# Kernel tuning notes

Hardware: AMD Instinct MI355X
Metric: run time of the kernel (lower is better)

## Reference

```python
import jax, jax.numpy as jnp
import numpy as np

E = 1024
H = 16
HD = E // H  # 64
R = 8
ALPHA = 32
SCALING = ALPHA / R  # LoRA scaling = 4.0


def _lora_linear(x, W, b, A, B):
    # x: [..., in], W: [out, in], A: [r, in], B: [out, r]
    base = jnp.einsum('...i,oi->...o', x, W) + b
    lora = jnp.einsum('...r,or->...o', jnp.einsum('...i,ri->...r', x, A), B) * SCALING
    return base + lora


def setup_inputs() -> dict:
    key = jax.random.key(0)
    ks = jax.random.split(key, 20)
    L, N = 2048, 2
    d = {}
    d['query'] = jax.random.normal(ks[0], (L, N, E), dtype=jnp.float32)
    d['key_padding_mask'] = jax.random.randint(ks[1], (N, L), 0, 2) > 0
    i = 2
    for p in ('q', 'k', 'v', 'o'):
        d['W' + p] = jax.random.normal(ks[i], (E, E), dtype=jnp.float32) * (E ** -0.5); i += 1
        d['b' + p] = jax.random.normal(ks[i], (E,), dtype=jnp.float32) * 0.01; i += 1
        d['A' + p] = jax.random.normal(ks[i], (R, E), dtype=jnp.float32) * (E ** -0.5); i += 1
        d['B' + p] = jax.random.normal(ks[i], (E, R), dtype=jnp.float32) * 0.01; i += 1
    return d


def reference(query, key_padding_mask, Wq, bq, Aq, Bq, Wk, bk, Ak, Bk,
              Wv, bv, Av, Bv, Wo, bo, Ao, Bo):
    L, N, _ = query.shape
    q = _lora_linear(query, Wq, bq, Aq, Bq)  # [L, N, E]
    k = _lora_linear(query, Wk, bk, Ak, Bk)
    v = _lora_linear(query, Wv, bv, Av, Bv)

    def split_heads(x):  # [L, N, E] -> [N, H, L, HD]
        return x.transpose(1, 0, 2).reshape(N, L, H, HD).transpose(0, 2, 1, 3)

    scale = HD ** -0.5
    qh = split_heads(q) * scale
    kh = split_heads(k)
    vh = split_heads(v)

    logits = jnp.einsum('nhqd,nhkd->nhqk', qh, kh)  # [N, H, L, L]
    dt = logits.dtype
    pad = key_padding_mask[:, None, None, :]  # [N, 1, 1, Lk]
    logits = jnp.where(pad, jnp.finfo(dt).min, logits)
    logits = logits - jnp.max(logits, axis=-1, keepdims=True)
    w = jax.nn.softmax(logits, axis=-1)
    # zero out padded keys then renormalize (faithful to the module)
    w = jnp.where(pad, jnp.zeros((), dt), w)
    denom = jnp.maximum(jnp.sum(w, axis=-1, keepdims=True), jnp.finfo(dt).tiny)
    w = w / denom

    out = jnp.einsum('nhqk,nhkd->nhqd', w, vh)  # [N, H, L, HD]
    out = out.transpose(0, 2, 1, 3).reshape(N, L, E).transpose(1, 0, 2)  # [L, N, E]
    attn_output = _lora_linear(out, Wo, bo, Ao, Bo)

    # average_attn_weights=True path: mean over heads, then permute(1,0,2)
    attn_weights_out = jnp.mean(w, axis=1).transpose(1, 0, 2)  # [Lq, N, Lk]
    return attn_output, attn_weights_out
```

## Files before the change

### kernel.cpp

```cpp
#include <hip/hip_runtime.h>
#include <stdint.h>


typedef __attribute__((ext_vector_type(8))) short short8;
typedef __attribute__((ext_vector_type(4))) float f32x4;

#define LORA_SCALING 4.0f
#define FTINY 1.1754943508222875e-38f

static __device__ __forceinline__ unsigned short f2bf(float f){
  unsigned u = __float_as_uint(f);
  u += 0x7fffu + ((u >> 16) & 1u);
  return (unsigned short)(u >> 16);
}
static __device__ __forceinline__ float bflo(unsigned u){ return __uint_as_float(u << 16); }
static __device__ __forceinline__ float bfhi(unsigned u){ return __uint_as_float(u & 0xffff0000u); }
static __device__ __forceinline__ unsigned pk2(float lo, float hi){
  return (unsigned)f2bf(lo) | ((unsigned)f2bf(hi) << 16);
}

union S8U { short8 v; uint2 u[2]; };

__global__ __launch_bounds__(256) void pack_bf16(const float* __restrict__ src,
                                                 unsigned short* __restrict__ dst)
{
  const size_t i = (size_t)blockIdx.x * 256 + threadIdx.x;
  const float4 f0 = ((const float4*)src)[i*2];
  const float4 f1 = ((const float4*)src)[i*2 + 1];
  ((uint4*)dst)[i] = make_uint4(pk2(f0.x,f0.y), pk2(f0.z,f0.w),
                                pk2(f1.x,f1.y), pk2(f1.z,f1.w));
}

__global__ __launch_bounds__(256) void xa_kernel(const unsigned short* __restrict__ X,
                                                 const float* __restrict__ A,
                                                 float* __restrict__ xa)
{
  __shared__ float red[4][8];
  const int t = blockIdx.x, tid = threadIdx.x;
  const int lane = tid & 63, wid = tid >> 6;

  const uint2 xr = *(const uint2*)(X + (size_t)t*1024 + tid*4);
  const float x0 = bflo(xr.x), x1 = bfhi(xr.x), x2 = bflo(xr.y), x3 = bfhi(xr.y);

  float acc[8];
#pragma unroll
  for (int r = 0; r < 8; ++r) {
    const float4 ar = *(const float4*)(A + (size_t)r*1024 + tid*4);
    acc[r] = x0*ar.x + x1*ar.y + x2*ar.z + x3*ar.w;
  }
#pragma unroll
  for (int r = 0; r < 8; ++r) {
    float v = acc[r];
#pragma unroll
    for (int off = 32; off > 0; off >>= 1) v += __shfl_xor(v, off, 64);
    if (lane == 0) red[wid][r] = v;
  }
  __syncthreads();
  if (tid < 8) xa[(size_t)t*8 + tid] = red[0][tid] + red[1][tid] + red[2][tid] + red[3][tid];
}

__global__ __launch_bounds__(256) void gemm_bf16(
    const unsigned short* __restrict__ Abf,
    const unsigned short* __restrict__ W0bf, const unsigned short* __restrict__ W1bf,
    const unsigned short* __restrict__ W2bf,
    const float* __restrict__ B0, const float* __restrict__ B1, const float* __restrict__ B2,
    const float* __restrict__ xa0, const float* __restrict__ xa1, const float* __restrict__ xa2,
    const float* __restrict__ L0, const float* __restrict__ L1, const float* __restrict__ L2,
    void* __restrict__ C0, void* __restrict__ C1, void* __restrict__ C2,
    int fp32out)
{
  const int z = blockIdx.z;
  const unsigned short* W = (z==0)?W0bf:((z==1)?W1bf:W2bf);
  const float* Bb = (z==0)?B0:((z==1)?B1:B2);
  const float* xa = (z==0)?xa0:((z==1)?xa1:xa2);
  const float* Lb = (z==0)?L0:((z==1)?L1:L2);
  void*        C  = (z==0)?C0:((z==1)?C1:C2);
  const bool vtw = (z == 2);

  __shared__ alignas(16) unsigned short As[128*32];
  __shared__ alignas(16) unsigned short Bs[128*32];

  const int tid = threadIdx.x;
  const int lane = tid & 63, wid = tid >> 6;
  const int quad = lane >> 4, lm = lane & 15;
  const int t0 = blockIdx.x * 128, n0 = blockIdx.y * 128;
  const int wm = (wid & 1) * 64, wn = (wid >> 1) * 64;

  const int srow = tid >> 1;
  const int shalf = (tid & 1) * 16;

  f32x4 acc[4][4];
#pragma unroll
  for (int i = 0; i < 4; ++i)
#pragma unroll
    for (int j = 0; j < 4; ++j) acc[i][j] = 0.f;

  for (int kt = 0; kt < 32; ++kt) {
    const int k0 = kt * 32;
    const unsigned short* ga = Abf + (size_t)(t0 + srow)*1024 + k0 + shalf;
    const uint4 a0 = *(const uint4*)ga;
    const uint4 a1 = *(const uint4*)(ga + 8);
    const unsigned short* gb = W + (size_t)(n0 + srow)*1024 + k0 + shalf;
    const uint4 b0 = *(const uint4*)gb;
    const uint4 b1 = *(const uint4*)(gb + 8);
    __syncthreads();
    *(uint4*)&As[srow*32 + shalf]     = a0;
    *(uint4*)&As[srow*32 + shalf + 8] = a1;
    *(uint4*)&Bs[srow*32 + shalf]     = b0;
    *(uint4*)&Bs[srow*32 + shalf + 8] = b1;
    __syncthreads();
    short8 a[4], b[4];
#pragma unroll
    for (int i = 0; i < 4; ++i) a[i] = *(const short8*)&As[(wm + i*16 + lm)*32 + quad*8];
#pragma unroll
    for (int j = 0; j < 4; ++j) b[j] = *(const short8*)&Bs[(wn + j*16 + lm)*32 + quad*8];
#pragma unroll
    for (int i = 0; i < 4; ++i)
#pragma unroll
      for (int j = 0; j < 4; ++j)
        acc[i][j] = __builtin_amdgcn_mfma_f32_16x16x32_bf16(a[i], b[j], acc[i][j], 0, 0, 0);
  }

#pragma unroll
  for (int j = 0; j < 4; ++j) {
    const int col = n0 + wn + j*16 + lm;
    const float bias = Bb[col];
    const float4 u0 = ((const float4*)(Lb + (size_t)col*8))[0];
    const float4 u1 = ((const float4*)(Lb + (size_t)col*8))[1];
#pragma unroll
    for (int i = 0; i < 4; ++i) {
#pragma unroll
      for (int r = 0; r < 4; ++r) {
        const int row = t0 + wm + i*16 + quad*4 + r;
        const float* xr = xa + (size_t)row*8;
        const float lora = xr[0]*u0.x + xr[1]*u0.y + xr[2]*u0.z + xr[3]*u0.w
                         + xr[4]*u1.x + xr[5]*u1.y + xr[6]*u1.z + xr[7]*u1.w;
        const float val = acc[i][j][r] + bias + LORA_SCALING*lora;
        if (fp32out) {
          ((float*)C)[(size_t)row*1024 + col] = val;
        } else if (vtw) {
          ((unsigned short*)C)[((size_t)(row & 1) * 1024 + col) * 2048 + (row >> 1)] = f2bf(val);
        } else {
          ((unsigned short*)C)[(size_t)row*1024 + col] = f2bf(val);
        }
      }
    }
  }
}

__global__ __launch_bounds__(256) void attn_pv(
    const unsigned short* __restrict__ qb, const unsigned short* __restrict__ kb,
    const unsigned short* __restrict__ vt, const int* __restrict__ mask,
    unsigned short* __restrict__ ctx, float* __restrict__ msl)
{
  __shared__ alignas(16) unsigned short Es[128*132];
  __shared__ unsigned char mlds[2048];
  __shared__ float lred[2][128];

  const int tid = threadIdx.x, lane = tid & 63, wid = tid >> 6;
  const int quad = lane >> 4, lm = lane & 15;
  const int q0 = blockIdx.x * 128, n = blockIdx.y, h = blockIdx.z;
  const int wq = wid >> 1, wj = wid & 1;

  {
    const int4 m0 = *(const int4*)(mask + n*2048 + tid*8);
    const int4 m1 = *(const int4*)(mask + n*2048 + tid*8 + 4);
    mlds[tid*8+0] = (m0.x != 0); mlds[tid*8+1] = (m0.y != 0);
    mlds[tid*8+2] = (m0.z != 0); mlds[tid*8+3] = (m0.w != 0);
    mlds[tid*8+4] = (m1.x != 0); mlds[tid*8+5] = (m1.y != 0);
    mlds[tid*8+6] = (m1.z != 0); mlds[tid*8+7] = (m1.w != 0);
  }

  short8 bq[4][2];
#pragma unroll
  for (int q_t = 0; q_t < 4; ++q_t) {
    const unsigned short* qg = qb + ((size_t)(q0 + wq*64 + q_t*16 + lm)*2 + n)*1024 + h*64 + quad*8;
    bq[q_t][0] = *(const short8*)qg;
    bq[q_t][1] = *(const short8*)(qg + 32);
  }

  float lsum[4] = {0.f, 0.f, 0.f, 0.f};
  f32x4 oacc[2][4];
#pragma unroll
  for (int i2 = 0; i2 < 2; ++i2)
#pragma unroll
    for (int dt = 0; dt < 4; ++dt) oacc[i2][dt] = 0.f;

  for (int jt = 0; jt < 16; ++jt) {
    const int j0 = jt * 128;
    __syncthreads();

    f32x4 sacc[4][4];
#pragma unroll
    for (int a = 0; a < 4; ++a)
#pragma unroll
      for (int b = 0; b < 4; ++b) sacc[a][b] = 0.f;
#pragma unroll
    for (int kt = 0; kt < 2; ++kt) {
      short8 ak[4];
#pragma unroll
      for (int j_t = 0; j_t < 4; ++j_t)
        ak[j_t] = *(const short8*)(kb + ((size_t)(j0 + wj*64 + j_t*16 + lm)*2 + n)*1024 + h*64 + kt*32 + quad*8);
#pragma unroll
      for (int j_t = 0; j_t < 4; ++j_t)
#pragma unroll
        for (int q_t = 0; q_t < 4; ++q_t)
          sacc[j_t][q_t] = __builtin_amdgcn_mfma_f32_16x16x32_bf16(ak[j_t], bq[q_t][kt], sacc[j_t][q_t], 0, 0, 0);
    }
#pragma unroll
    for (int j_t = 0; j_t < 4; ++j_t) {
      const int jrow = wj*64 + j_t*16 + quad*4;
      const uchar4 mk = *(const uchar4*)&mlds[j0 + jrow];
#pragma unroll
      for (int q_t = 0; q_t < 4; ++q_t) {
        const float e0 = mk.x ? 0.f : __expf(sacc[j_t][q_t][0]*0.125f);
        const float e1 = mk.y ? 0.f : __expf(sacc[j_t][q_t][1]*0.125f);
        const float e2 = mk.z ? 0.f : __expf(sacc[j_t][q_t][2]*0.125f);
        const float e3 = mk.w ? 0.f : __expf(sacc[j_t][q_t][3]*0.125f);
        lsum[q_t] += (e0 + e1) + (e2 + e3);
        const int qcol = wq*64 + q_t*16 + lm;
        *(uint2*)&Es[qcol*132 + jrow] = make_uint2(pk2(e0, e1), pk2(e2, e3));
      }
    }
    __syncthreads();
#pragma unroll
    for (int kk = 0; kk < 4; ++kk) {
      S8U ae0, ae1;
      const int r0 = wid*32 + lm, r1 = r0 + 16;
      ae0.u[0] = *(const uint2*)&Es[r0*132 + kk*32 + quad*8];
      ae0.u[1] = *(const uint2*)&Es[r0*132 + kk*32 + quad*8 + 4];
      ae1.u[0] = *(const uint2*)&Es[r1*132 + kk*32 + quad*8];
      ae1.u[1] = *(const uint2*)&Es[r1*132 + kk*32 + quad*8 + 4];
      const unsigned short* vbase = vt + (size_t)((n*16 + h)*64)*2048 + j0 + kk*32 + quad*8;
#pragma unroll
      for (int dt = 0; dt < 4; ++dt) {
        const short8 bv = *(const short8*)(vbase + (size_t)(dt*16 + lm)*2048);
        oacc[0][dt] = __builtin_amdgcn_mfma_f32_16x16x32_bf16(ae0.v, bv, oacc[0][dt], 0, 0, 0);
        oacc[1][dt] = __builtin_amdgcn_mfma_f32_16x16x32_bf16(ae1.v, bv, oacc[1][dt], 0, 0, 0);
      }
    }
  }

#pragma unroll
  for (int q_t = 0; q_t < 4; ++q_t) {
    float v = lsum[q_t];
    v += __shfl_xor(v, 16, 64);
    v += __shfl_xor(v, 32, 64);
    if (quad == 0) lred[wj][wq*64 + q_t*16 + lm] = v;
  }
  __syncthreads();
  if (tid < 128) {
    const float l = lred[0][tid] + lred[1][tid];
    const float rinv = 1.0f / fmaxf(l, FTINY);
    lred[0][tid] = rinv;
    msl[(size_t)(h*2 + n)*2048 + q0 + tid] = rinv;
  }
  __syncthreads();
#pragma unroll
  for (int i2 = 0; i2 < 2; ++i2) {
    const int rb = wid*32 + i2*16 + quad*4;
    const float4 rv4 = *(const float4*)&lred[0][rb];
    const float rva[4] = {rv4.x, rv4.y, rv4.z, rv4.w};
#pragma unroll
    for (int dt = 0; dt < 4; ++dt) {
#pragma unroll
      for (int r = 0; r < 4; ++r) {
        ctx[((size_t)(q0 + rb + r)*2 + n)*1024 + h*64 + dt*16 + lm] =
            f2bf(oacc[i2][dt][r] * rva[r]);
      }
    }
  }
}

__global__ __launch_bounds__(256) void wmean2(
    const unsigned short* __restrict__ qb, const unsigned short* __restrict__ kb,
    const int* __restrict__ mask, const float* __restrict__ msl,
    float* __restrict__ wout)
{
  const int tid = threadIdx.x, lane = tid & 63, wid = tid >> 6;
  const int quad = lane >> 4, lm = lane & 15;
  const int q0 = blockIdx.x * 128, j0 = blockIdx.y * 128, n = blockIdx.z;
  const int wq = wid >> 1, wj = wid & 1;

  unsigned fm = 0;
#pragma unroll
  for (int j_t = 0; j_t < 4; ++j_t)
    fm |= (mask[n*2048 + j0 + wj*64 + j_t*16 + lm] != 0 ? 1u : 0u) << j_t;

  f32x4 wacc[4][4];
#pragma unroll
  for (int i = 0; i < 4; ++i)
#pragma unroll
    for (int j = 0; j < 4; ++j) wacc[i][j] = 0.f;

  for (int h = 0; h < 16; ++h) {
    short8 aq[4][2];
#pragma unroll
    for (int i = 0; i < 4; ++i) {
      const unsigned short* qg = qb + ((size_t)(q0 + wq*64 + i*16 + lm)*2 + n)*1024 + h*64 + quad*8;
      aq[i][0] = *(const short8*)qg;
      aq[i][1] = *(const short8*)(qg + 32);
    }
    float4 rv[4];
#pragma unroll
    for (int i = 0; i < 4; ++i)
      rv[i] = *(const float4*)&msl[(size_t)(h*2 + n)*2048 + q0 + wq*64 + i*16 + quad*4];
#pragma unroll
    for (int jh2 = 0; jh2 < 2; ++jh2) {
      short8 bk[2][2];
#pragma unroll
      for (int jtl = 0; jtl < 2; ++jtl) {
        const unsigned short* kg = kb + ((size_t)(j0 + wj*64 + (jh2*2 + jtl)*16 + lm)*2 + n)*1024 + h*64 + quad*8;
        bk[jtl][0] = *(const short8*)kg;
        bk[jtl][1] = *(const short8*)(kg + 32);
      }
      f32x4 sacc[4][2];
#pragma unroll
      for (int i = 0; i < 4; ++i)
#pragma unroll
        for (int jtl = 0; jtl < 2; ++jtl) sacc[i][jtl] = 0.f;
#pragma unroll
      for (int kt = 0; kt < 2; ++kt)
#pragma unroll
        for (int i = 0; i < 4; ++i)
#pragma unroll
          for (int jtl = 0; jtl < 2; ++jtl)
            sacc[i][jtl] = __builtin_amdgcn_mfma_f32_16x16x32_bf16(aq[i][kt], bk[jtl][kt], sacc[i][jtl], 0, 0, 0);
#pragma unroll
      for (int i = 0; i < 4; ++i) {
        const float rva[4] = {rv[i].x, rv[i].y, rv[i].z, rv[i].w};
#pragma unroll
        for (int jtl = 0; jtl < 2; ++jtl) {
          const int j_t = jh2*2 + jtl;
          const bool mskd = (fm >> j_t) & 1u;
#pragma unroll
          for (int r = 0; r < 4; ++r) {
            const float e = mskd ? 0.f : __expf(sacc[i][jtl][r]*0.125f) * rva[r];
            wacc[i][j_t][r] += e;
          }
        }
      }
    }
  }
#pragma unroll
  for (int i = 0; i < 4; ++i)
#pragma unroll
    for (int j_t = 0; j_t < 4; ++j_t)
#pragma unroll
      for (int r = 0; r < 4; ++r) {
        const int row = q0 + wq*64 + i*16 + quad*4 + r;
        const int col = j0 + wj*64 + j_t*16 + lm;
        wout[((size_t)row*2 + n)*2048 + col] = wacc[i][j_t][r] * 0.0625f;
      }
}

__global__ __launch_bounds__(256) void ctx_copy(const uint4* __restrict__ src,
                                                uint4* __restrict__ dst)
{
  const size_t i = (size_t)blockIdx.x * 256 + threadIdx.x;
  dst[i] = src[i];
}

extern "C" void kernel_launch(void* const* d_in, const int* in_sizes, int n_in,
                              void* d_out, int out_size, void* d_ws, size_t ws_size,
                              hipStream_t stream) {
  const float* x    = (const float*)d_in[0];
  const int*   mask = (const int*)d_in[1];
  const float* Wq = (const float*)d_in[2];  const float* bq = (const float*)d_in[3];
  const float* Aq = (const float*)d_in[4];  const float* Bq = (const float*)d_in[5];
  const float* Wk = (const float*)d_in[6];  const float* bk = (const float*)d_in[7];
  const float* Ak = (const float*)d_in[8];  const float* Bk = (const float*)d_in[9];
  const float* Wv = (const float*)d_in[10]; const float* bv = (const float*)d_in[11];
  const float* Av = (const float*)d_in[12]; const float* Bv = (const float*)d_in[13];
  const float* Wo = (const float*)d_in[14]; const float* bo = (const float*)d_in[15];
  const float* Ao = (const float*)d_in[16]; const float* Bo = (const float*)d_in[17];

  float* outF = (float*)d_out;
  float* woutF = outF + 4194304;

  unsigned short* kbuf = (unsigned short*)d_ws;
  unsigned short* vtb  = kbuf + 4194304;
  unsigned short* qbuf = vtb  + 4194304;

  float* xaq = woutF;
  float* xak = xaq + 32768;
  float* xav = xak + 32768;

  unsigned short* Xbf  = (unsigned short*)outF;
  unsigned short* Wqbf = (unsigned short*)(outF + 2097152);
  unsigned short* Wkbf = (unsigned short*)(outF + 2621440);
  unsigned short* Wvbf = (unsigned short*)(outF + 3145728);
  unsigned short* ctx16 = (unsigned short*)outF;
  float* msl = outF + 2359296;

  float* xao = (float*)vtb;
  unsigned short* Wobf = vtb + 524288;

  pack_bf16<<<dim3(2048), dim3(256), 0, stream>>>(x, Xbf);
  pack_bf16<<<dim3(512),  dim3(256), 0, stream>>>(Wq, Wqbf);
  pack_bf16<<<dim3(512),  dim3(256), 0, stream>>>(Wk, Wkbf);
  pack_bf16<<<dim3(512),  dim3(256), 0, stream>>>(Wv, Wvbf);

  xa_kernel<<<dim3(4096), dim3(256), 0, stream>>>(Xbf, Aq, xaq);
  xa_kernel<<<dim3(4096), dim3(256), 0, stream>>>(Xbf, Ak, xak);
  xa_kernel<<<dim3(4096), dim3(256), 0, stream>>>(Xbf, Av, xav);

  gemm_bf16<<<dim3(32, 8, 3), dim3(256), 0, stream>>>(
      Xbf, Wqbf, Wkbf, Wvbf, bq, bk, bv, xaq, xak, xav, Bq, Bk, Bv,
      qbuf, kbuf, vtb, 0);

  attn_pv<<<dim3(16, 2, 16), dim3(256), 0, stream>>>(qbuf, kbuf, vtb, mask, ctx16, msl);

  pack_bf16<<<dim3(512), dim3(256), 0, stream>>>(Wo, Wobf);

  wmean2<<<dim3(16, 16, 2), dim3(256), 0, stream>>>(qbuf, kbuf, mask, msl, woutF);

  ctx_copy<<<dim3(2048), dim3(256), 0, stream>>>((const uint4*)ctx16, (uint4*)kbuf);

  xa_kernel<<<dim3(4096), dim3(256), 0, stream>>>(kbuf, Ao, xao);

  gemm_bf16<<<dim3(32, 8, 1), dim3(256), 0, stream>>>(
      kbuf, Wobf, Wobf, Wobf, bo, bo, bo, xao, xao, xao, Bo, Bo, Bo,
      outF, outF, outF, 1);
}
```

Baseline: 496.9 us.

## Halve query tile in attention kernels to double grid size and occupancy

Shrinks the query tile from 128 to 64 rows in both attn_pv and wmean2, doubling the grid, rebalancing warps in attn_pv (each warp now owns 32 keys for QK and 16 query rows for PV, with a 4-way lsum reduction), and adding a min-blocks launch bound of 4. It also swaps the software bf16 rounding for the hardware v_cvt_pk_bf16_f32 instruction when packing the exp values. The aim is more waves per CU and better latency hiding, since the original grid was only 512 blocks. The cost is that K and V tiles are reloaded twice as often, and per-block work is smaller.

```diff
diff --git a/kernel.cpp b/kernel.cpp
--- a/kernel.cpp
+++ b/kernel.cpp
@@ -17,6 +17,11 @@
 static __device__ __forceinline__ float bfhi(unsigned u){ return __uint_as_float(u & 0xffff0000u); }
 static __device__ __forceinline__ unsigned pk2(float lo, float hi){
   return (unsigned)f2bf(lo) | ((unsigned)f2bf(hi) << 16);
+}
+static __device__ __forceinline__ unsigned cvtpk(float lo, float hi){
+  unsigned r;
+  asm("v_cvt_pk_bf16_f32 %0, %1, %2" : "=v"(r) : "v"(lo), "v"(hi));
+  return r;
 }
 
 union S8U { short8 v; uint2 u[2]; };
@@ -148,19 +153,18 @@
   }
 }
 
-__global__ __launch_bounds__(256) void attn_pv(
+__global__ __launch_bounds__(256, 4) void attn_pv(
     const unsigned short* __restrict__ qb, const unsigned short* __restrict__ kb,
     const unsigned short* __restrict__ vt, const int* __restrict__ mask,
     unsigned short* __restrict__ ctx, float* __restrict__ msl)
 {
-  __shared__ alignas(16) unsigned short Es[128*132];
+  __shared__ alignas(16) unsigned short Es[64*132];
   __shared__ unsigned char mlds[2048];
-  __shared__ float lred[2][128];
+  __shared__ float lred[4][64];
 
   const int tid = threadIdx.x, lane = tid & 63, wid = tid >> 6;
   const int quad = lane >> 4, lm = lane & 15;
-  const int q0 = blockIdx.x * 128, n = blockIdx.y, h = blockIdx.z;
-  const int wq = wid >> 1, wj = wid & 1;
+  const int q0 = blockIdx.x * 64, n = blockIdx.y, h = blockIdx.z;
 
   {
     const int4 m0 = *(const int4*)(mask + n*2048 + tid*8);
@@ -174,42 +178,40 @@
   short8 bq[4][2];
 #pragma unroll
   for (int q_t = 0; q_t < 4; ++q_t) {
-    const unsigned short* qg = qb + ((size_t)(q0 + wq*64 + q_t*16 + lm)*2 + n)*1024 + h*64 + quad*8;
+    const unsigned short* qg = qb + ((size_t)(q0 + q_t*16 + lm)*2 + n)*1024 + h*64 + quad*8;
     bq[q_t][0] = *(const short8*)qg;
     bq[q_t][1] = *(const short8*)(qg + 32);
   }
 
   float lsum[4] = {0.f, 0.f, 0.f, 0.f};
-  f32x4 oacc[2][4];
-#pragma unroll
-  for (int i2 = 0; i2 < 2; ++i2)
-#pragma unroll
-    for (int dt = 0; dt < 4; ++dt) oacc[i2][dt] = 0.f;
+  f32x4 oacc[4];
+#pragma unroll
+  for (int dt = 0; dt < 4; ++dt) oacc[dt] = 0.f;
 
   for (int jt = 0; jt < 16; ++jt) {
     const int j0 = jt * 128;
     __syncthreads();
 
-    f32x4 sacc[4][4];
-#pragma unroll
-    for (int a = 0; a < 4; ++a)
+    f32x4 sacc[2][4];
+#pragma unroll
+    for (int a = 0; a < 2; ++a)
 #pragma unroll
       for (int b = 0; b < 4; ++b) sacc[a][b] = 0.f;
 #pragma unroll
     for (int kt = 0; kt < 2; ++kt) {
-      short8 ak[4];
-#pragma unroll
-      for (int j_t = 0; j_t < 4; ++j_t)
-        ak[j_t] = *(const short8*)(kb + ((size_t)(j0 + wj*64 + j_t*16 + lm)*2 + n)*1024 + h*64 + kt*32 + quad*8);
-#pragma unroll
-      for (int j_t = 0; j_t < 4; ++j_t)
+      short8 ak[2];
+#pragma unroll
+      for (int j_t = 0; j_t < 2; ++j_t)
+        ak[j_t] = *(const short8*)(kb + ((size_t)(j0 + wid*32 + j_t*16 + lm)*2 + n)*1024 + h*64 + kt*32 + quad*8);
+#pragma unroll
+      for (int j_t = 0; j_t < 2; ++j_t)
 #pragma unroll
         for (int q_t = 0; q_t < 4; ++q_t)
           sacc[j_t][q_t] = __builtin_amdgcn_mfma_f32_16x16x32_bf16(ak[j_t], bq[q_t][kt], sacc[j_t][q_t], 0, 0, 0);
     }
 #pragma unroll
-    for (int j_t = 0; j_t < 4; ++j_t) {
-      const int jrow = wj*64 + j_t*16 + quad*4;
+    for (int j_t = 0; j_t < 2; ++j_t) {
+      const int jrow = wid*32 + j_t*16 + quad*4;
       const uchar4 mk = *(const uchar4*)&mlds[j0 + jrow];
 #pragma unroll
       for (int q_t = 0; q_t < 4; ++q_t) {
@@ -218,25 +220,22 @@
         const float e2 = mk.z ? 0.f : __expf(sacc[j_t][q_t][2]*0.125f);
         const float e3 = mk.w ? 0.f : __expf(sacc[j_t][q_t][3]*0.125f);
         lsum[q_t] += (e0 + e1) + (e2 + e3);
-        const int qcol = wq*64 + q_t*16 + lm;
-        *(uint2*)&Es[qcol*132 + jrow] = make_uint2(pk2(e0, e1), pk2(e2, e3));
+        const int qcol = q_t*16 + lm;
+        *(uint2*)&Es[qcol*132 + jrow] = make_uint2(cvtpk(e0, e1), cvtpk(e2, e3));
       }
     }
     __syncthreads();
 #pragma unroll
     for (int kk = 0; kk < 4; ++kk) {
-      S8U ae0, ae1;
-      const int r0 = wid*32 + lm, r1 = r0 + 16;
-      ae0.u[0] = *(const uint2*)&Es[r0*132 + kk*32 + quad*8];
-      ae0.u[1] = *(const uint2*)&Es[r0*132 + kk*32 + quad*8 + 4];
-      ae1.u[0] = *(const uint2*)&Es[r1*132 + kk*32 + quad*8];
-      ae1.u[1] = *(const uint2*)&Es[r1*132 + kk*32 + quad*8 + 4];
+      S8U ae;
+      const int r0 = wid*16 + lm;
+      ae.u[0] = *(const uint2*)&Es[r0*132 + kk*32 + quad*8];
+      ae.u[1] = *(const uint2*)&Es[r0*132 + kk*32 + quad*8 + 4];
       const unsigned short* vbase = vt + (size_t)((n*16 + h)*64)*2048 + j0 + kk*32 + quad*8;
 #pragma unroll
       for (int dt = 0; dt < 4; ++dt) {
         const short8 bv = *(const short8*)(vbase + (size_t)(dt*16 + lm)*2048);
-        oacc[0][dt] = __builtin_amdgcn_mfma_f32_16x16x32_bf16(ae0.v, bv, oacc[0][dt], 0, 0, 0);
-        oacc[1][dt] = __builtin_amdgcn_mfma_f32_16x16x32_bf16(ae1.v, bv, oacc[1][dt], 0, 0, 0);
+        oacc[dt] = __builtin_amdgcn_mfma_f32_16x16x32_bf16(ae.v, bv, oacc[dt], 0, 0, 0);
       }
     }
   }
@@ -246,19 +245,18 @@
     float v = lsum[q_t];
     v += __shfl_xor(v, 16, 64);
     v += __shfl_xor(v, 32, 64);
-    if (quad == 0) lred[wj][wq*64 + q_t*16 + lm] = v;
+    if (quad == 0) lred[wid][q_t*16 + lm] = v;
   }
   __syncthreads();
-  if (tid < 128) {
-    const float l = lred[0][tid] + lred[1][tid];
+  if (tid < 64) {
+    const float l = lred[0][tid] + lred[1][tid] + lred[2][tid] + lred[3][tid];
     const float rinv = 1.0f / fmaxf(l, FTINY);
     lred[0][tid] = rinv;
     msl[(size_t)(h*2 + n)*2048 + q0 + tid] = rinv;
   }
   __syncthreads();
-#pragma unroll
-  for (int i2 = 0; i2 < 2; ++i2) {
-    const int rb = wid*32 + i2*16 + quad*4;
+  {
+    const int rb = wid*16 + quad*4;
     const float4 rv4 = *(const float4*)&lred[0][rb];
     const float rva[4] = {rv4.x, rv4.y, rv4.z, rv4.w};
 #pragma unroll
@@ -266,20 +264,20 @@
 #pragma unroll
       for (int r = 0; r < 4; ++r) {
         ctx[((size_t)(q0 + rb + r)*2 + n)*1024 + h*64 + dt*16 + lm] =
-            f2bf(oacc[i2][dt][r] * rva[r]);
-      }
-    }
-  }
-}
-
-__global__ __launch_bounds__(256) void wmean2(
+            f2bf(oacc[dt][r] * rva[r]);
+      }
+    }
+  }
+}
+
+__global__ __launch_bounds__(256, 4) void wmean2(
     const unsigned short* __restrict__ qb, const unsigned short* __restrict__ kb,
     const int* __restrict__ mask, const float* __restrict__ msl,
     float* __restrict__ wout)
 {
   const int tid = threadIdx.x, lane = tid & 63, wid = tid >> 6;
   const int quad = lane >> 4, lm = lane & 15;
-  const int q0 = blockIdx.x * 128, j0 = blockIdx.y * 128, n = blockIdx.z;
+  const int q0 = blockIdx.x * 64, j0 = blockIdx.y * 128, n = blockIdx.z;
   const int wq = wid >> 1, wj = wid & 1;
 
   unsigned fm = 0;
@@ -287,24 +285,24 @@
   for (int j_t = 0; j_t < 4; ++j_t)
     fm |= (mask[n*2048 + j0 + wj*64 + j_t*16 + lm] != 0 ? 1u : 0u) << j_t;
 
-  f32x4 wacc[4][4];
-#pragma unroll
-  for (int i = 0; i < 4; ++i)
+  f32x4 wacc[2][4];
+#pragma unroll
+  for (int i = 0; i < 2; ++i)
 #pragma unroll
     for (int j = 0; j < 4; ++j) wacc[i][j] = 0.f;
 
   for (int h = 0; h < 16; ++h) {
-    short8 aq[4][2];
-#pragma unroll
-    for (int i = 0; i < 4; ++i) {
-      const unsigned short* qg = qb + ((size_t)(q0 + wq*64 + i*16 + lm)*2 + n)*1024 + h*64 + quad*8;
+    short8 aq[2][2];
+#pragma unroll
+    for (int i = 0; i < 2; ++i) {
+      const unsigned short* qg = qb + ((size_t)(q0 + wq*32 + i*16 + lm)*2 + n)*1024 + h*64 + quad*8;
       aq[i][0] = *(const short8*)qg;
       aq[i][1] = *(const short8*)(qg + 32);
     }
-    float4 rv[4];
-#pragma unroll
-    for (int i = 0; i < 4; ++i)
-      rv[i] = *(const float4*)&msl[(size_t)(h*2 + n)*2048 + q0 + wq*64 + i*16 + quad*4];
+    float4 rv[2];
+#pragma unroll
+    for (int i = 0; i < 2; ++i)
+      rv[i] = *(const float4*)&msl[(size_t)(h*2 + n)*2048 + q0 + wq*32 + i*16 + quad*4];
 #pragma unroll
     for (int jh2 = 0; jh2 < 2; ++jh2) {
       short8 bk[2][2];
@@ -314,20 +312,20 @@
         bk[jtl][0] = *(const short8*)kg;
         bk[jtl][1] = *(const short8*)(kg + 32);
       }
-      f32x4 sacc[4][2];
-#pragma unroll
-      for (int i = 0; i < 4; ++i)
+      f32x4 sacc[2][2];
+#pragma unroll
+      for (int i = 0; i < 2; ++i)
 #pragma unroll
         for (int jtl = 0; jtl < 2; ++jtl) sacc[i][jtl] = 0.f;
 #pragma unroll
       for (int kt = 0; kt < 2; ++kt)
 #pragma unroll
-        for (int i = 0; i < 4; ++i)
+        for (int i = 0; i < 2; ++i)
 #pragma unroll
           for (int jtl = 0; jtl < 2; ++jtl)
             sacc[i][jtl] = __builtin_amdgcn_mfma_f32_16x16x32_bf16(aq[i][kt], bk[jtl][kt], sacc[i][jtl], 0, 0, 0);
 #pragma unroll
-      for (int i = 0; i < 4; ++i) {
+      for (int i = 0; i < 2; ++i) {
         const float rva[4] = {rv[i].x, rv[i].y, rv[i].z, rv[i].w};
 #pragma unroll
         for (int jtl = 0; jtl < 2; ++jtl) {
@@ -343,12 +341,12 @@
     }
   }
 #pragma unroll
-  for (int i = 0; i < 4; ++i)
+  for (int i = 0; i < 2; ++i)
 #pragma unroll
     for (int j_t = 0; j_t < 4; ++j_t)
 #pragma unroll
       for (int r = 0; r < 4; ++r) {
-        const int row = q0 + wq*64 + i*16 + quad*4 + r;
+        const int row = q0 + wq*32 + i*16 + quad*4 + r;
         const int col = j0 + wj*64 + j_t*16 + lm;
         wout[((size_t)row*2 + n)*2048 + col] = wacc[i][j_t][r] * 0.0625f;
       }
@@ -409,11 +407,11 @@
       Xbf, Wqbf, Wkbf, Wvbf, bq, bk, bv, xaq, xak, xav, Bq, Bk, Bv,
       qbuf, kbuf, vtb, 0);
 
-  attn_pv<<<dim3(16, 2, 16), dim3(256), 0, stream>>>(qbuf, kbuf, vtb, mask, ctx16, msl);
+  attn_pv<<<dim3(32, 2, 16), dim3(256), 0, stream>>>(qbuf, kbuf, vtb, mask, ctx16, msl);
 
   pack_bf16<<<dim3(512), dim3(256), 0, stream>>>(Wo, Wobf);
 
-  wmean2<<<dim3(16, 16, 2), dim3(256), 0, stream>>>(qbuf, kbuf, mask, msl, woutF);
+  wmean2<<<dim3(32, 16, 2), dim3(256), 0, stream>>>(qbuf, kbuf, mask, msl, woutF);
 
   ctx_copy<<<dim3(2048), dim3(256), 0, stream>>>((const uint4*)ctx16, (uint4*)kbuf);
 
```

Measured after the change: 542.5 us. 1.09x slower.

## Load GEMM tiles directly to LDS, fold softmax scale into Q projection

Applied to the files above, without the earlier changes.

The projection GEMM now stages A and W tiles with global_load_lds (direct global-to-LDS 16-byte loads) instead of loading into registers and then storing to shared memory. The 1/sqrt(head_dim) scale is applied in the Q projection epilogue, which removes a multiply per logit in both attention kernels. The attention kernel also packs bf16 with the hardware v_cvt_pk_bf16_f32 instruction instead of software rounding. Scaling Q before bf16 rounding changes rounding slightly, and the direct-to-LDS loads still sit between barriers with no double buffering.

```diff
diff --git a/kernel.cpp b/kernel.cpp
--- a/kernel.cpp
+++ b/kernel.cpp
@@ -17,6 +17,16 @@
 static __device__ __forceinline__ float bfhi(unsigned u){ return __uint_as_float(u & 0xffff0000u); }
 static __device__ __forceinline__ unsigned pk2(float lo, float hi){
   return (unsigned)f2bf(lo) | ((unsigned)f2bf(hi) << 16);
+}
+static __device__ __forceinline__ unsigned cvtpk(float lo, float hi){
+  unsigned r;
+  asm("v_cvt_pk_bf16_f32 %0, %1, %2" : "=v"(r) : "v"(lo), "v"(hi));
+  return r;
+}
+static __device__ __forceinline__ void gload16(const void* g, void* l){
+  __builtin_amdgcn_global_load_lds(
+      (const __attribute__((address_space(1))) unsigned int*)g,
+      (__attribute__((address_space(3))) unsigned int*)l, 16, 0, 0);
 }
 
 union S8U { short8 v; uint2 u[2]; };
@@ -67,7 +77,7 @@
     const float* __restrict__ xa0, const float* __restrict__ xa1, const float* __restrict__ xa2,
     const float* __restrict__ L0, const float* __restrict__ L1, const float* __restrict__ L2,
     void* __restrict__ C0, void* __restrict__ C1, void* __restrict__ C2,
-    int fp32out)
+    int fp32out, float scale0)
 {
   const int z = blockIdx.z;
   const unsigned short* W = (z==0)?W0bf:((z==1)?W1bf:W2bf);
@@ -76,6 +86,7 @@
   const float* Lb = (z==0)?L0:((z==1)?L1:L2);
   void*        C  = (z==0)?C0:((z==1)?C1:C2);
   const bool vtw = (z == 2);
+  const float sc = (z == 0) ? scale0 : 1.0f;
 
   __shared__ alignas(16) unsigned short As[128*32];
   __shared__ alignas(16) unsigned short Bs[128*32];
@@ -86,8 +97,9 @@
   const int t0 = blockIdx.x * 128, n0 = blockIdx.y * 128;
   const int wm = (wid & 1) * 64, wn = (wid >> 1) * 64;
 
-  const int srow = tid >> 1;
-  const int shalf = (tid & 1) * 16;
+  const int c0 = tid, c1 = tid + 256;
+  const int r0c = c0 >> 2, e0c = (c0 & 3) * 8;
+  const int r1c = c1 >> 2, e1c = (c1 & 3) * 8;
 
   f32x4 acc[4][4];
 #pragma unroll
@@ -97,17 +109,11 @@
 
   for (int kt = 0; kt < 32; ++kt) {
     const int k0 = kt * 32;
-    const unsigned short* ga = Abf + (size_t)(t0 + srow)*1024 + k0 + shalf;
-    const uint4 a0 = *(const uint4*)ga;
-    const uint4 a1 = *(const uint4*)(ga + 8);
-    const unsigned short* gb = W + (size_t)(n0 + srow)*1024 + k0 + shalf;
-    const uint4 b0 = *(const uint4*)gb;
-    const uint4 b1 = *(const uint4*)(gb + 8);
     __syncthreads();
-    *(uint4*)&As[srow*32 + shalf]     = a0;
-    *(uint4*)&As[srow*32 + shalf + 8] = a1;
-    *(uint4*)&Bs[srow*32 + shalf]     = b0;
-    *(uint4*)&Bs[srow*32 + shalf + 8] = b1;
+    gload16(Abf + (size_t)(t0 + r0c)*1024 + k0 + e0c, &As[c0*8]);
+    gload16(Abf + (size_t)(t0 + r1c)*1024 + k0 + e1c, &As[c1*8]);
+    gload16(W   + (size_t)(n0 + r0c)*1024 + k0 + e0c, &Bs[c0*8]);
+    gload16(W   + (size_t)(n0 + r1c)*1024 + k0 + e1c, &Bs[c1*8]);
     __syncthreads();
     short8 a[4], b[4];
 #pragma unroll
@@ -135,7 +141,7 @@
         const float* xr = xa + (size_t)row*8;
         const float lora = xr[0]*u0.x + xr[1]*u0.y + xr[2]*u0.z + xr[3]*u0.w
                          + xr[4]*u1.x + xr[5]*u1.y + xr[6]*u1.z + xr[7]*u1.w;
-        const float val = acc[i][j][r] + bias + LORA_SCALING*lora;
+        const float val = (acc[i][j][r] + bias + LORA_SCALING*lora) * sc;
         if (fp32out) {
           ((float*)C)[(size_t)row*1024 + col] = val;
         } else if (vtw) {
@@ -213,13 +219,13 @@
       const uchar4 mk = *(const uchar4*)&mlds[j0 + jrow];
 #pragma unroll
       for (int q_t = 0; q_t < 4; ++q_t) {
-        const float e0 = mk.x ? 0.f : __expf(sacc[j_t][q_t][0]*0.125f);
-        const float e1 = mk.y ? 0.f : __expf(sacc[j_t][q_t][1]*0.125f);
-        const float e2 = mk.z ? 0.f : __expf(sacc[j_t][q_t][2]*0.125f);
-        const float e3 = mk.w ? 0.f : __expf(sacc[j_t][q_t][3]*0.125f);
+        const float e0 = mk.x ? 0.f : __expf(sacc[j_t][q_t][0]);
+        const float e1 = mk.y ? 0.f : __expf(sacc[j_t][q_t][1]);
+        const float e2 = mk.z ? 0.f : __expf(sacc[j_t][q_t][2]);
+        const float e3 = mk.w ? 0.f : __expf(sacc[j_t][q_t][3]);
         lsum[q_t] += (e0 + e1) + (e2 + e3);
         const int qcol = wq*64 + q_t*16 + lm;
-        *(uint2*)&Es[qcol*132 + jrow] = make_uint2(pk2(e0, e1), pk2(e2, e3));
+        *(uint2*)&Es[qcol*132 + jrow] = make_uint2(cvtpk(e0, e1), cvtpk(e2, e3));
       }
     }
     __syncthreads();
@@ -335,7 +341,7 @@
           const bool mskd = (fm >> j_t) & 1u;
 #pragma unroll
           for (int r = 0; r < 4; ++r) {
-            const float e = mskd ? 0.f : __expf(sacc[i][jtl][r]*0.125f) * rva[r];
+            const float e = mskd ? 0.f : __expf(sacc[i][jtl][r]) * rva[r];
             wacc[i][j_t][r] += e;
           }
         }
@@ -407,7 +413,7 @@
 
   gemm_bf16<<<dim3(32, 8, 3), dim3(256), 0, stream>>>(
       Xbf, Wqbf, Wkbf, Wvbf, bq, bk, bv, xaq, xak, xav, Bq, Bk, Bv,
-      qbuf, kbuf, vtb, 0);
+      qbuf, kbuf, vtb, 0, 0.125f);
 
   attn_pv<<<dim3(16, 2, 16), dim3(256), 0, stream>>>(qbuf, kbuf, vtb, mask, ctx16, msl);
 
@@ -421,5 +427,5 @@
 
   gemm_bf16<<<dim3(32, 8, 1), dim3(256), 0, stream>>>(
       kbuf, Wobf, Wobf, Wobf, bo, bo, bo, xao, xao, xao, Bo, Bo, Bo,
-      outF, outF, outF, 1);
-}
+      outF, outF, outF, 1, 1.0f);
+}
```

Result: faster. 472.5 us (-4.9%).
